# Performance work log

Measured on AMD Instinct MI355X. Metric: run time of the kernel, lower is better.

Reference implementation:

```python
import jax, jax.numpy as jnp
import numpy as np

SIGMA = 1.5
KSIZE = 3
CROP = 5

def _gaussian_window():
    # matches cv2.getGaussianKernel(3, 1.5): normalized 1D gaussian, outer product
    g = np.exp(-((np.arange(KSIZE) - (KSIZE - 1) / 2.0) ** 2) / (2.0 * SIGMA ** 2))
    g = g / g.sum()
    return np.outer(g, g)  # (3, 3)

def _filt(img, win):
    # img: [B, W, H, C]; 3x3 depthwise correlation with BORDER_REFLECT_101 (= jnp 'reflect')
    C = img.shape[-1]
    p = jnp.pad(img, ((0, 0), (1, 1), (1, 1), (0, 0)), mode='reflect')
    k = jnp.broadcast_to(win[:, :, None, None], (KSIZE, KSIZE, 1, C)).astype(img.dtype)
    return jax.lax.conv_general_dilated(
        p, k, window_strides=(1, 1), padding='VALID',
        dimension_numbers=('NHWC', 'HWIO', 'NHWC'), feature_group_count=C)

def setup_inputs() -> dict:
    key = jax.random.key(0)
    k1, k2 = jax.random.split(key)
    X = jax.random.uniform(k1, (32, 3, 512, 512), dtype=jnp.float32) * 255.0
    Y = jax.random.uniform(k2, (32, 3, 512, 512), dtype=jnp.float32) * 255.0
    return {"X": X, "Y": Y}

def reference(X, Y):
    B, C, W, H = X.shape
    # source does numpy reshape (c,w,h)->(w,h,c); replicate exactly
    x = X.reshape(B, W, H, C)
    y = Y.reshape(B, W, H, C)
    win = jnp.asarray(_gaussian_window(), dtype=X.dtype)
    c = slice(CROP, -CROP)
    mu1 = _filt(x, win)[:, c, c, :]
    mu2 = _filt(y, win)[:, c, c, :]
    sigma1_sq = _filt(x * x, win)[:, c, c, :] - mu1 * mu1
    sigma2_sq = _filt(y * y, win)[:, c, c, :] - mu2 * mu2
    sigma12 = _filt(x * y, win)[:, c, c, :] - mu1 * mu2
    loss = sigma1_sq + sigma2_sq - 2.0 * sigma12  # local variance of (x - y)
    return jnp.sum(jnp.mean(loss, axis=(1, 2, 3)))
```

## Files before the change

### kernel.cpp

```cpp
#include <hip/hip_runtime.h>

constexpr int Bn     = 32;
constexpr int Wd     = 512;
constexpr int Hd     = 512;
constexpr int Cd     = 3;
constexpr int CROPc  = 5;
constexpr int NOUTc  = Wd - 2 * CROPc;
constexpr int HCc    = NOUTc * Cd;
constexpr int NCHUNK = 8;
constexpr int CHUNKc = (NOUTc + NCHUNK - 1) / NCHUNK;
constexpr int BLOCK  = 256;
constexpr int TOTAL  = Bn * NCHUNK * HCc;
constexpr int NBLK   = TOTAL / BLOCK;
static_assert(TOTAL % BLOCK == 0, "grid must be exact");


__global__ __launch_bounds__(BLOCK) void locvar_kernel(
    const float* __restrict__ X,
    const float* __restrict__ Y,
    float* __restrict__ partial)
{
    const int tid   = blockIdx.x * BLOCK + threadIdx.x;
    const int hcidx = tid % HCc;
    const int outer = tid / HCc;
    const int chunk = outer % NCHUNK;
    const int b     = outer / NCHUNK;

    const int h  = CROPc + hcidx / Cd;
    const int c  = hcidx % Cd;
    const int w0 = CROPc + chunk * CHUNKc;
    const int wn = min(CHUNKc, CROPc + NOUTc - w0);

    const float e  = expf(-1.0f / 4.5f);
    const float g1 = 1.0f / (1.0f + 2.0f * e);
    const float g0 = e * g1;

    const size_t rowstride = (size_t)Hd * Cd;
    const size_t base = (size_t)b * Wd * rowstride + (size_t)h * Cd + c;

    float R0, R1, Q0, Q1;
    {
        size_t off = base + (size_t)(w0 - 1) * rowstride;
        float dm = X[off - 3] - Y[off - 3];
        float d0 = X[off]     - Y[off];
        float dp = X[off + 3] - Y[off + 3];
        R0 = g0 * (dm + dp) + g1 * d0;
        Q0 = g0 * (dm * dm + dp * dp) + g1 * (d0 * d0);
    }
    {
        size_t off = base + (size_t)w0 * rowstride;
        float dm = X[off - 3] - Y[off - 3];
        float d0 = X[off]     - Y[off];
        float dp = X[off + 3] - Y[off + 3];
        R1 = g0 * (dm + dp) + g1 * d0;
        Q1 = g0 * (dm * dm + dp * dp) + g1 * (d0 * d0);
    }

    float acc = 0.0f;
    size_t off = base + (size_t)(w0 + 1) * rowstride;
    for (int i = 0; i < wn; ++i, off += rowstride) {
        float dm = X[off - 3] - Y[off - 3];
        float d0 = X[off]     - Y[off];
        float dp = X[off + 3] - Y[off + 3];
        float R2 = g0 * (dm + dp) + g1 * d0;
        float Q2 = g0 * (dm * dm + dp * dp) + g1 * (d0 * d0);

        float S1 = g0 * (R0 + R2) + g1 * R1;
        float S2 = g0 * (Q0 + Q2) + g1 * Q1;
        acc += S2 - S1 * S1;

        R0 = R1; R1 = R2;
        Q0 = Q1; Q1 = Q2;
    }

    #pragma unroll
    for (int o = 32; o > 0; o >>= 1) acc += __shfl_down(acc, o, 64);

    __shared__ float sdata[BLOCK / 64];
    const int lane = threadIdx.x & 63;
    const int wid  = threadIdx.x >> 6;
    if (lane == 0) sdata[wid] = acc;
    __syncthreads();
    if (threadIdx.x == 0) {
        float s = 0.0f;
        #pragma unroll
        for (int i = 0; i < BLOCK / 64; ++i) s += sdata[i];
        partial[blockIdx.x] = s;
    }
}

__global__ __launch_bounds__(BLOCK) void reduce_kernel(
    const float* __restrict__ partial,
    float* __restrict__ out)
{
    float acc = 0.0f;
    for (int i = threadIdx.x; i < NBLK; i += BLOCK) acc += partial[i];

    #pragma unroll
    for (int o = 32; o > 0; o >>= 1) acc += __shfl_down(acc, o, 64);

    __shared__ float sdata[BLOCK / 64];
    const int lane = threadIdx.x & 63;
    const int wid  = threadIdx.x >> 6;
    if (lane == 0) sdata[wid] = acc;
    __syncthreads();
    if (threadIdx.x == 0) {
        float s = 0.0f;
        #pragma unroll
        for (int i = 0; i < BLOCK / 64; ++i) s += sdata[i];
        out[0] = s * (1.0f / ((float)NOUTc * (float)NOUTc * (float)Cd));
    }
}

extern "C" void kernel_launch(void* const* d_in, const int* in_sizes, int n_in,
                              void* d_out, int out_size, void* d_ws, size_t ws_size,
                              hipStream_t stream) {
    const float* X = (const float*)d_in[0];
    const float* Y = (const float*)d_in[1];
    float* out     = (float*)d_out;
    float* partial = (float*)d_ws;

    locvar_kernel<<<NBLK, BLOCK, 0, stream>>>(X, Y, partial);
    reduce_kernel<<<1, BLOCK, 0, stream>>>(partial, out);
}
```

Before: 41.92 us.

## Share horizontal neighbors via wave lane permutes instead of redundant loads

Each wavefront now covers 64 contiguous h*c positions with a 3-lane halo on each side. Every lane loads one X/Y pair per row and gets its -3/+3 neighbors through ds_bpermute, where before it issued three separate loads per row. Halo lanes and out-of-range positions are masked out of the accumulation, and the chunk size and work mapping are changed to match. This cuts global load instructions to a third in exchange for two cross-lane permutes per row and about 10% idle lanes.

```diff
diff --git a/kernel.cpp b/kernel.cpp
--- a/kernel.cpp
+++ b/kernel.cpp
@@ -1,85 +1,93 @@
 #include <hip/hip_runtime.h>
 
-constexpr int Bn     = 32;
+
 constexpr int Wd     = 512;
 constexpr int Hd     = 512;
 constexpr int Cd     = 3;
+constexpr int ROW    = Hd * Cd;
 constexpr int CROPc  = 5;
 constexpr int NOUTc  = Wd - 2 * CROPc;
-constexpr int HCc    = NOUTc * Cd;
+constexpr int HC_LO  = 15;
+constexpr int HC_HI  = 1520;
+constexpr int OUT_PER_WAVE = 58;
+constexpr int NHCW   = (NOUTc * Cd + OUT_PER_WAVE - 1) / OUT_PER_WAVE;
 constexpr int NCHUNK = 8;
-constexpr int CHUNKc = (NOUTc + NCHUNK - 1) / NCHUNK;
+constexpr int CHUNKc = 63;
 constexpr int BLOCK  = 256;
-constexpr int TOTAL  = Bn * NCHUNK * HCc;
-constexpr int NBLK   = TOTAL / BLOCK;
-static_assert(TOTAL % BLOCK == 0, "grid must be exact");
-
+constexpr int NWAVES = 32 * NCHUNK * NHCW;
+constexpr int NBLK   = NWAVES / (BLOCK / 64);
+static_assert(NWAVES % (BLOCK / 64) == 0, "");
 
 __global__ __launch_bounds__(BLOCK) void locvar_kernel(
     const float* __restrict__ X,
     const float* __restrict__ Y,
     float* __restrict__ partial)
 {
-    const int tid   = blockIdx.x * BLOCK + threadIdx.x;
-    const int hcidx = tid % HCc;
-    const int outer = tid / HCc;
-    const int chunk = outer % NCHUNK;
-    const int b     = outer / NCHUNK;
+    const int lane = threadIdx.x & 63;
+    const int widx = threadIdx.x >> 6;
+    const int gw   = blockIdx.x * (BLOCK / 64) + widx;
 
-    const int h  = CROPc + hcidx / Cd;
-    const int c  = hcidx % Cd;
+    const int hcw   = gw % NHCW;
+    const int rest  = gw / NHCW;
+    const int chunk = rest % NCHUNK;
+    const int b     = rest / NCHUNK;
+
+    const int hc = 12 + OUT_PER_WAVE * hcw + lane;
     const int w0 = CROPc + chunk * CHUNKc;
     const int wn = min(CHUNKc, CROPc + NOUTc - w0);
+
+    const bool valid = (lane >= 3) && (lane <= 60) && (hc >= HC_LO) && (hc <= HC_HI);
+    const float vmask = valid ? 1.0f : 0.0f;
 
     const float e  = expf(-1.0f / 4.5f);
     const float g1 = 1.0f / (1.0f + 2.0f * e);
     const float g0 = e * g1;
 
-    const size_t rowstride = (size_t)Hd * Cd;
-    const size_t base = (size_t)b * Wd * rowstride + (size_t)h * Cd + c;
+    const int am = ((lane - 3) & 63) << 2;
+    const int ap = ((lane + 3) & 63) << 2;
+
+    const size_t base = (size_t)b * Wd * ROW + (size_t)hc;
+
+#define ROWSUMS(OFF, Rr, Qq)                                                     \
+    {                                                                            \
+        float dd  = X[(OFF)] - Y[(OFF)];                                         \
+        float dmv = __int_as_float(                                              \
+            __builtin_amdgcn_ds_bpermute(am, __float_as_int(dd)));               \
+        float dpv = __int_as_float(                                              \
+            __builtin_amdgcn_ds_bpermute(ap, __float_as_int(dd)));               \
+        Rr = g0 * (dmv + dpv) + g1 * dd;                                         \
+        Qq = g0 * fmaf(dpv, dpv, dmv * dmv) + g1 * (dd * dd);                    \
+    }
 
     float R0, R1, Q0, Q1;
     {
-        size_t off = base + (size_t)(w0 - 1) * rowstride;
-        float dm = X[off - 3] - Y[off - 3];
-        float d0 = X[off]     - Y[off];
-        float dp = X[off + 3] - Y[off + 3];
-        R0 = g0 * (dm + dp) + g1 * d0;
-        Q0 = g0 * (dm * dm + dp * dp) + g1 * (d0 * d0);
-    }
-    {
-        size_t off = base + (size_t)w0 * rowstride;
-        float dm = X[off - 3] - Y[off - 3];
-        float d0 = X[off]     - Y[off];
-        float dp = X[off + 3] - Y[off + 3];
-        R1 = g0 * (dm + dp) + g1 * d0;
-        Q1 = g0 * (dm * dm + dp * dp) + g1 * (d0 * d0);
+        size_t off = base + (size_t)(w0 - 1) * ROW;
+        ROWSUMS(off, R0, Q0);
+        off += ROW;
+        ROWSUMS(off, R1, Q1);
     }
 
     float acc = 0.0f;
-    size_t off = base + (size_t)(w0 + 1) * rowstride;
-    for (int i = 0; i < wn; ++i, off += rowstride) {
-        float dm = X[off - 3] - Y[off - 3];
-        float d0 = X[off]     - Y[off];
-        float dp = X[off + 3] - Y[off + 3];
-        float R2 = g0 * (dm + dp) + g1 * d0;
-        float Q2 = g0 * (dm * dm + dp * dp) + g1 * (d0 * d0);
+    size_t off = base + (size_t)(w0 + 1) * ROW;
+    #pragma unroll 2
+    for (int i = 0; i < wn; ++i, off += ROW) {
+        float R2, Q2;
+        ROWSUMS(off, R2, Q2);
 
         float S1 = g0 * (R0 + R2) + g1 * R1;
         float S2 = g0 * (Q0 + Q2) + g1 * Q1;
-        acc += S2 - S1 * S1;
+        acc += vmask * fmaf(-S1, S1, S2);
 
         R0 = R1; R1 = R2;
         Q0 = Q1; Q1 = Q2;
     }
+#undef ROWSUMS
 
     #pragma unroll
     for (int o = 32; o > 0; o >>= 1) acc += __shfl_down(acc, o, 64);
 
     __shared__ float sdata[BLOCK / 64];
-    const int lane = threadIdx.x & 63;
-    const int wid  = threadIdx.x >> 6;
-    if (lane == 0) sdata[wid] = acc;
+    if (lane == 0) sdata[widx] = acc;
     __syncthreads();
     if (threadIdx.x == 0) {
         float s = 0.0f;
```

New measurement: 42.48 us. Within noise of the previous version (+1.3%).
